# Optimization experiments

Hardware: AMD Instinct MI355X
Metric: run time of the kernel (lower is better)

## Reference

```python
import jax, jax.numpy as jnp
import numpy as np

B, T, E_DIM, H, J, V = 32, 1000, 512, 512, 512, 1024
BLANK = 0

def setup_inputs() -> dict:
    key = jax.random.key(0)
    ks = jax.random.split(key, 8)
    s = lambda k, shp, sc: jax.random.normal(k, shp, jnp.float32) * sc
    return {
        "encoder_output": jax.random.normal(ks[0], (B, T, E_DIM), jnp.float32),
        "embed": s(ks[1], (V, H), 0.02),
        "W_ih": s(ks[2], (H, 4 * H), 0.05),
        "W_hh": s(ks[3], (H, 4 * H), 0.05),
        "b_lstm": jnp.zeros((4 * H,), jnp.float32),
        "W_enc": s(ks[4], (E_DIM, J), 0.05),
        "W_dec": s(ks[5], (H, J), 0.05),
        "b_joint": jnp.zeros((J,), jnp.float32),
        "W_out": s(ks[6], (J, V), 0.05),
    }

def _lstm_step(tok, h, c, embed, W_ih, W_hh, b):
    # prediction network: embedding lookup + single-layer LSTM cell
    x = embed[tok]                                   # [B, H]
    gates = x @ W_ih + h @ W_hh + b                  # [B, 4H]
    i, f, g, o = jnp.split(gates, 4, axis=-1)
    c_new = jax.nn.sigmoid(f) * c + jax.nn.sigmoid(i) * jnp.tanh(g)
    h_new = jax.nn.sigmoid(o) * jnp.tanh(c_new)
    return h_new, c_new

def reference(encoder_output, embed, W_ih, W_hh, b_lstm, W_enc, W_dec, b_joint, W_out):
    # transducer_greedy_decode (beam_size <= 1 path), vectorized over batch,
    # sequential over encoder time steps via lax.scan.
    Bv = encoder_output.shape[0]
    h0 = jnp.zeros((Bv, H), encoder_output.dtype)
    c0 = jnp.zeros((Bv, H), encoder_output.dtype)
    tok0 = jnp.full((Bv,), BLANK, jnp.int32)
    # initial decoder call on blank token with zero hidden
    out_PN0, c1 = _lstm_step(tok0, h0, c0, embed, W_ih, W_hh, b_lstm)
    # precompute encoder projection of the joint (same math, one big GEMM)
    enc_proj = encoder_output @ W_enc                # [B, T, J]

    def step(carry, enc_t):
        out_PN, h, c, score = carry
        logits = jnp.tanh(enc_t + out_PN @ W_dec + b_joint) @ W_out   # [B, V]
        logp = jax.nn.log_softmax(logits, axis=-1)
        lp = jnp.max(logp, axis=-1)                  # best log-prob
        pos = jnp.argmax(logp, axis=-1)              # best token
        emit = pos != BLANK                          # hypotheses to update
        h_new, c_new = _lstm_step(pos.astype(jnp.int32), h, c, embed, W_ih, W_hh, b_lstm)
        m = emit[:, None]
        out_PN = jnp.where(m, h_new, out_PN)
        h = jnp.where(m, h_new, h)
        c = jnp.where(m, c_new, c)
        score = score + jnp.where(emit, lp, 0.0)
        tok = jnp.where(emit, pos, BLANK)            # BLANK marks 'no emission'
        return (out_PN, h, c, score), tok

    init = (out_PN0, out_PN0, c1, jnp.zeros((Bv,), encoder_output.dtype))
    (_, _, _, scores), toks = jax.lax.scan(step, init, jnp.swapaxes(enc_proj, 0, 1))
    predictions = toks.T                             # [B, T], BLANK = no emission
    mean_exp_score = jnp.exp(scores).mean()
    return predictions, scores, mean_exp_score
```

## Files before the change

### kernel.cpp

```cpp
#include <hip/hip_runtime.h>
#include <math.h>

#define BB 32
#define TT 1000
#define HH 512
#define JJ 512
#define VV 1024
#define G4 2048
#define NB 128
#define NT 1024
#define NGRP 16
#define BPG (NB / NGRP)

#define RLX __ATOMIC_RELAXED
#define AGT __HIP_MEMORY_SCOPE_AGENT

__device__ __align__(16) float g_encp[(size_t)TT * JJ * BB];
__device__ __align__(16) float g_E[(size_t)VV * G4];
__device__ __align__(16) float g_h[HH * BB];
__device__ __align__(16) float g_c[BB * HH];
__device__ __align__(16) float g_joint[JJ * BB];
__device__ __align__(16) float g_hW[BB * G4];
__device__ float g_pm[BB * NB];
__device__ float g_ps[BB * NB];
__device__ int   g_pa[BB * NB];
__device__ float g_score[BB];
__device__ int g_cnt[3 * 1024];
__device__ int g_top[3 * 64];
__device__ int g_gen[3 * 1024];

__device__ __forceinline__ void gbar_arrive(int grp, int ph, int tp1) {
    __syncthreads();
    if (threadIdx.x == 0) {
        int p = __hip_atomic_fetch_add(&g_cnt[ph * 1024 + grp * 64], 1, RLX, AGT);
        if (p == tp1 * BPG - 1) {
            int q = __hip_atomic_fetch_add(&g_top[ph * 64], 1, RLX, AGT);
            if (q == tp1 * NGRP - 1) {
#pragma unroll
                for (int i = 0; i < NGRP; ++i)
                    __hip_atomic_store(&g_gen[ph * 1024 + i * 64], tp1, RLX, AGT);
            }
        }
    }
}
__device__ __forceinline__ void gbar_wait(int grp, int ph, int tp1) {
    if (threadIdx.x == 0) {
        while (__hip_atomic_load(&g_gen[ph * 1024 + grp * 64], RLX, AGT) < tp1)
            __builtin_amdgcn_s_sleep(1);
    }
    __syncthreads();
}

__global__ __launch_bounds__(256) void k_encproj(const float* __restrict__ enc,
                                                 const float* __restrict__ Wenc) {
    __shared__ __align__(16) float x[BB * 512];
    const int t = blockIdx.x;
    for (int i = threadIdx.x; i < BB * 128; i += 256) {
        const int b = i >> 7, k4 = i & 127;
        *reinterpret_cast<float4*>(x + b * 512 + k4 * 4) =
            *reinterpret_cast<const float4*>(enc + ((size_t)(b * TT + t)) * 512 + k4 * 4);
    }
    __syncthreads();
    const int j = threadIdx.x;
    float acc0[BB], acc1[BB];
#pragma unroll
    for (int b = 0; b < BB; ++b) { acc0[b] = 0.f; acc1[b] = 0.f; }
    for (int k4 = 0; k4 < 128; ++k4) {
        const int k = k4 * 4;
        float w0[4], w1[4];
#pragma unroll
        for (int i = 0; i < 4; ++i) {
            w0[i] = Wenc[(size_t)(k + i) * JJ + j];
            w1[i] = Wenc[(size_t)(k + i) * JJ + j + 256];
        }
#pragma unroll
        for (int b = 0; b < BB; ++b) {
            const float4 xv = *reinterpret_cast<const float4*>(x + b * 512 + k);
            acc0[b] += xv.x * w0[0] + xv.y * w0[1] + xv.z * w0[2] + xv.w * w0[3];
            acc1[b] += xv.x * w1[0] + xv.y * w1[1] + xv.z * w1[2] + xv.w * w1[3];
        }
    }
    float* outt = g_encp + (size_t)t * JJ * BB;
#pragma unroll
    for (int b = 0; b < BB; ++b) {
        outt[j * BB + b]         = acc0[b];
        outt[(j + 256) * BB + b] = acc1[b];
    }
}

__global__ __launch_bounds__(256) void k_embproj(const float* __restrict__ emb,
                                                 const float* __restrict__ Wih) {
    __shared__ __align__(16) float x[BB * 512];
    const int v0 = (blockIdx.x >> 2) * 32;
    const int g0 = (blockIdx.x & 3) * 512;
    for (int i = threadIdx.x; i < BB * 128; i += 256) {
        const int b = i >> 7, k4 = i & 127;
        *reinterpret_cast<float4*>(x + b * 512 + k4 * 4) =
            *reinterpret_cast<const float4*>(emb + (size_t)(v0 + b) * 512 + k4 * 4);
    }
    __syncthreads();
    const int j = g0 + threadIdx.x;
    float acc0[BB], acc1[BB];
#pragma unroll
    for (int b = 0; b < BB; ++b) { acc0[b] = 0.f; acc1[b] = 0.f; }
    for (int k4 = 0; k4 < 128; ++k4) {
        const int k = k4 * 4;
        float w0[4], w1[4];
#pragma unroll
        for (int i = 0; i < 4; ++i) {
            w0[i] = Wih[(size_t)(k + i) * G4 + j];
            w1[i] = Wih[(size_t)(k + i) * G4 + j + 256];
        }
#pragma unroll
        for (int b = 0; b < BB; ++b) {
            const float4 xv = *reinterpret_cast<const float4*>(x + b * 512 + k);
            acc0[b] += xv.x * w0[0] + xv.y * w0[1] + xv.z * w0[2] + xv.w * w0[3];
            acc1[b] += xv.x * w1[0] + xv.y * w1[1] + xv.z * w1[2] + xv.w * w1[3];
        }
    }
#pragma unroll
    for (int b = 0; b < BB; ++b) {
        g_E[(size_t)(v0 + b) * G4 + j]       = acc0[b];
        g_E[(size_t)(v0 + b) * G4 + j + 256] = acc1[b];
    }
}

__global__ void k_init(const float* __restrict__ bl) {
    const int k = threadIdx.x;
    const float ig = g_E[k]        + bl[k];
    const float gg = g_E[1024 + k] + bl[1024 + k];
    const float og = g_E[1536 + k] + bl[1536 + k];
    const float si = 1.f / (1.f + expf(-ig));
    const float so = 1.f / (1.f + expf(-og));
    const float c1 = si * tanhf(gg);
    const float h1 = so * tanhf(c1);
    for (int b = 0; b < BB; ++b) {
        g_h[k * BB + b] = h1;
        g_c[b * HH + k] = c1;
    }
    if (k < BB) g_score[k] = 0.f;
    for (int i = k; i < 3 * 1024; i += 512) { g_cnt[i] = 0; g_gen[i] = 0; }
    if (k < 3 * 64) g_top[k] = 0;
}

template<int KN>
__device__ __forceinline__ void mv4(const float* __restrict__ w_lds, const int wpad,
                                    const int c0, const int k0,
                                    const float* __restrict__ x_lds,
                                    const int ks, const int b4, float acc[4][4]) {
#pragma unroll
    for (int c = 0; c < 4; ++c)
#pragma unroll
        for (int r = 0; r < 4; ++r) acc[c][r] = 0.f;
#pragma unroll 8
    for (int i = 0; i < KN; ++i) {
        const int k = k0 + i * 8 + ks;
        const float4 xv = *reinterpret_cast<const float4*>(x_lds + k * 32 + b4 * 4);
        const float4 wv = *reinterpret_cast<const float4*>(w_lds + k * wpad + c0);
        acc[0][0] += wv.x * xv.x; acc[0][1] += wv.x * xv.y; acc[0][2] += wv.x * xv.z; acc[0][3] += wv.x * xv.w;
        acc[1][0] += wv.y * xv.x; acc[1][1] += wv.y * xv.y; acc[1][2] += wv.y * xv.z; acc[1][3] += wv.y * xv.w;
        acc[2][0] += wv.z * xv.x; acc[2][1] += wv.z * xv.y; acc[2][2] += wv.z * xv.z; acc[2][3] += wv.z * xv.w;
        acc[3][0] += wv.w * xv.x; acc[3][1] += wv.w * xv.y; acc[3][2] += wv.w * xv.z; acc[3][3] += wv.w * xv.w;
    }
#pragma unroll
    for (int off = 8; off <= 32; off <<= 1)
#pragma unroll
        for (int c = 0; c < 4; ++c)
#pragma unroll
            for (int r = 0; r < 4; ++r) acc[c][r] += __shfl_xor(acc[c][r], off, 64);
}

__global__ __launch_bounds__(NT) void k_loop(const float* __restrict__ Wdec,
                                             const float* __restrict__ Wout,
                                             const float* __restrict__ Whh,
                                             const float* __restrict__ bj,
                                             const float* __restrict__ bl,
                                             float* __restrict__ out) {
    __shared__ __align__(16) float x_lds[512 * 32];
    __shared__ __align__(16) float wab_lds[512 * 20];
    __shared__ __align__(16) float wout_lds[512 * 12];
    __shared__ float part_lds[2 * 160];
    __shared__ float logit_lds[8 * 33];
    __shared__ float red_m[2], red_s[2];
    __shared__ int   red_a[2];

    const int blk = blockIdx.x, tid = threadIdx.x;
    const int grp = blk & (NGRP - 1);
    const int wv = tid >> 6, lane = tid & 63, ks = lane >> 3, b4 = lane & 7;

    for (int i = tid; i < 512 * 20; i += NT) {
        const int k = i / 20, c = i - k * 20;
        wab_lds[i] = (c < 16) ? Whh[(size_t)k * G4 + blk * 16 + c]
                              : Wdec[(size_t)k * JJ + blk * 4 + (c - 16)];
    }
    for (int i = tid; i < 512 * 12; i += NT) {
        const int k = i / 12, c = i - k * 12;
        wout_lds[i] = (c < 8) ? Wout[(size_t)k * VV + blk * 8 + c] : 0.f;
    }
    float bjr[4];
#pragma unroll
    for (int c = 0; c < 4; ++c) bjr[c] = bj[blk * 4 + c];
    __syncthreads();

    float acc[4][4];
    for (int t = 0; t < TT; ++t) {
        {
            float v[16];
#pragma unroll
            for (int p = 0; p < 16; ++p)
                v[p] = __hip_atomic_load(&g_h[tid + p * 1024], RLX, AGT);
#pragma unroll
            for (int p = 0; p < 16; ++p) x_lds[tid + p * 1024] = v[p];
        }
        __syncthreads();
        if (wv < 4) {
            mv4<64>(wab_lds, 20, wv * 4, 0, x_lds, ks, b4, acc);
            if (ks == 0) {
#pragma unroll
                for (int c = 0; c < 4; ++c)
#pragma unroll
                    for (int j = 0; j < 4; ++j)
                        __hip_atomic_store(&g_hW[(size_t)(b4 * 4 + j) * G4 + blk * 16 + wv * 4 + c],
                                           acc[c][j], RLX, AGT);
            }
        } else if (wv < 6) {
            mv4<32>(wab_lds, 20, 16, (wv - 4) * 256, x_lds, ks, b4, acc);
            if (wv == 5 && ks == 0) {
#pragma unroll
                for (int c = 0; c < 4; ++c)
#pragma unroll
                    for (int j = 0; j < 4; ++j)
                        part_lds[c * 33 + b4 * 4 + j] = acc[c][j];
            }
        }
        __syncthreads();
        if (wv == 4 && ks == 0) {
            const float* ep = g_encp + (size_t)t * JJ * BB + (size_t)blk * 4 * BB;
#pragma unroll
            for (int c = 0; c < 4; ++c) {
                const float4 ev = *reinterpret_cast<const float4*>(ep + c * BB + b4 * 4);
                const float evv[4] = { ev.x, ev.y, ev.z, ev.w };
#pragma unroll
                for (int j = 0; j < 4; ++j) {
                    const float u = acc[c][j] + part_lds[c * 33 + b4 * 4 + j] + evv[j] + bjr[c];
                    __hip_atomic_store(&g_joint[(blk * 4 + c) * BB + b4 * 4 + j],
                                       tanhf(u), RLX, AGT);
                }
            }
        }
        gbar_arrive(grp, 0, t + 1);
        gbar_wait(grp, 0, t + 1);

        {
            float v[16];
#pragma unroll
            for (int p = 0; p < 16; ++p)
                v[p] = __hip_atomic_load(&g_joint[tid + p * 1024], RLX, AGT);
#pragma unroll
            for (int p = 0; p < 16; ++p) x_lds[tid + p * 1024] = v[p];
        }
        __syncthreads();
        if (wv < 4) {
            const int tile = wv & 1, kh = wv >> 1;
            mv4<32>(wout_lds, 12, tile * 4, kh * 256, x_lds, ks, b4, acc);
            if (kh == 1 && ks == 0) {
#pragma unroll
                for (int c = 0; c < 4; ++c)
#pragma unroll
                    for (int j = 0; j < 4; ++j)
                        part_lds[tile * 160 + c * 33 + b4 * 4 + j] = acc[c][j];
            }
        }
        __syncthreads();
        if (wv < 2 && ks == 0) {
#pragma unroll
            for (int c = 0; c < 4; ++c)
#pragma unroll
                for (int j = 0; j < 4; ++j)
                    logit_lds[(wv * 4 + c) * 33 + b4 * 4 + j] =
                        acc[c][j] + part_lds[wv * 160 + c * 33 + b4 * 4 + j];
        }
        __syncthreads();
        if (wv == 0 && lane < BB) {
            const int b = lane;
            float m = -1e30f; int a = 0;
#pragma unroll
            for (int c = 0; c < 8; ++c) {
                const float l = logit_lds[c * 33 + b];
                if (l > m) { m = l; a = blk * 8 + c; }
            }
            float s = 0.f;
#pragma unroll
            for (int c = 0; c < 8; ++c) s += expf(logit_lds[c * 33 + b] - m);
            __hip_atomic_store(&g_pm[b * NB + blk], m, RLX, AGT);
            __hip_atomic_store(&g_pa[b * NB + blk], a, RLX, AGT);
            __hip_atomic_store(&g_ps[b * NB + blk], s, RLX, AGT);
        }
        gbar_arrive(grp, 1, t + 1);

        if (blk < BB) {
            gbar_wait(grp, 1, t + 1);
            const int r = blk;
            float m0 = -1e30f, s_loc = 0.f; int a0 = 1 << 30;
            if (tid < NB) {
                m0 = __hip_atomic_load(&g_pm[r * NB + tid], RLX, AGT);
                a0 = __hip_atomic_load(&g_pa[r * NB + tid], RLX, AGT);
                s_loc = __hip_atomic_load(&g_ps[r * NB + tid], RLX, AGT);
            }
            float m = m0; int a = a0;
#pragma unroll
            for (int off = 32; off; off >>= 1) {
                const float om = __shfl_xor(m, off, 64);
                const int   oa = __shfl_xor(a, off, 64);
                if (om > m || (om == m && oa < a)) { m = om; a = oa; }
            }
            if (lane == 0 && wv < 2) { red_m[wv] = m; red_a[wv] = a; }
            __syncthreads();
            float M; int P;
            {
                const float ma = red_m[0], mb = red_m[1];
                const int aa = red_a[0], ab = red_a[1];
                if (mb > ma || (mb == ma && ab < aa)) { M = mb; P = ab; }
                else { M = ma; P = aa; }
            }
            float e = (tid < NB) ? s_loc * expf(m0 - M) : 0.f;
#pragma unroll
            for (int off = 32; off; off >>= 1) e += __shfl_xor(e, off, 64);
            if (lane == 0 && wv < 2) red_s[wv] = e;
            __syncthreads();
            if (tid == 0) {
                const float S = red_s[0] + red_s[1];
                out[r * TT + t] = (float)P;
                if (P != 0) g_score[r] += -logf(S);
            }
            if (P != 0 && tid < HH) {
                const int k = tid;
                const float* Ep = g_E + (size_t)P * G4;
                const float hw0 = __hip_atomic_load(&g_hW[(size_t)r * G4 + k],        RLX, AGT);
                const float hw1 = __hip_atomic_load(&g_hW[(size_t)r * G4 + 512 + k],  RLX, AGT);
                const float hw2 = __hip_atomic_load(&g_hW[(size_t)r * G4 + 1024 + k], RLX, AGT);
                const float hw3 = __hip_atomic_load(&g_hW[(size_t)r * G4 + 1536 + k], RLX, AGT);
                const float i_g = Ep[k]        + hw0 + bl[k];
                const float f_g = Ep[512 + k]  + hw1 + bl[512 + k];
                const float g_g = Ep[1024 + k] + hw2 + bl[1024 + k];
                const float o_g = Ep[1536 + k] + hw3 + bl[1536 + k];
                const float si = 1.f / (1.f + expf(-i_g));
                const float sf = 1.f / (1.f + expf(-f_g));
                const float so = 1.f / (1.f + expf(-o_g));
                const float cn = sf * g_c[r * HH + k] + si * tanhf(g_g);
                const float hn = so * tanhf(cn);
                g_c[r * HH + k] = cn;
                __hip_atomic_store(&g_h[k * BB + r], hn, RLX, AGT);
            }
        }
        gbar_arrive(grp, 2, t + 1);
        gbar_wait(grp, 2, t + 1);
    }
}

__global__ void k_final(float* __restrict__ out) {
    const int b = threadIdx.x;
    float e = 0.f;
    if (b < BB) {
        const float sc = g_score[b];
        out[BB * TT + b] = sc;
        e = expf(sc);
    }
#pragma unroll
    for (int off = 32; off; off >>= 1) e += __shfl_xor(e, off, 64);
    if (b == 0) out[BB * TT + BB] = e / (float)BB;
}

extern "C" void kernel_launch(void* const* d_in, const int* in_sizes, int n_in,
                              void* d_out, int out_size, void* d_ws, size_t ws_size,
                              hipStream_t stream) {
    const float* enc  = (const float*)d_in[0];
    const float* emb  = (const float*)d_in[1];
    const float* Wih  = (const float*)d_in[2];
    const float* Whh  = (const float*)d_in[3];
    const float* bl   = (const float*)d_in[4];
    const float* Wenc = (const float*)d_in[5];
    const float* Wdec = (const float*)d_in[6];
    const float* bj   = (const float*)d_in[7];
    const float* Wout = (const float*)d_in[8];
    float* out = (float*)d_out;

    hipLaunchKernelGGL(k_encproj, dim3(TT), dim3(256), 0, stream, enc, Wenc);
    hipLaunchKernelGGL(k_embproj, dim3(128), dim3(256), 0, stream, emb, Wih);
    hipLaunchKernelGGL(k_init, dim3(1), dim3(512), 0, stream, bl);

    void* args[] = { (void*)&Wdec, (void*)&Wout, (void*)&Whh,
                     (void*)&bj, (void*)&bl, (void*)&out };
    hipLaunchCooperativeKernel((const void*)k_loop, dim3(NB), dim3(NT), args, 0, stream);

    hipLaunchKernelGGL(k_final, dim3(1), dim3(64), 0, stream, out);
}
```

Measured before the change: 28.17 ms.

## Replace hierarchical atomic grid barrier with flag-array barrier and spread LSTM update

Replaces the two-level counter-based grid barrier with a per-block flag array: each block writes its step number and then polls all 128 flags in parallel, taking the min with a block-wide reduction. This removes the serialized fetch_add chains and the generation broadcast. The LSTM update is now split across all 128 blocks (4 per batch row, each block doing 128 hidden units), where before only 32 blocks did it. Every block therefore repeats the argmax/logsumexp reduction for its row, and the W_dec matvec is spread over 4 waves with the encoder projection prefetched before the first sync. The cost is more polling traffic on 128 flags and redundant per-row reductions.

```diff
diff --git a/kernel.cpp b/kernel.cpp
--- a/kernel.cpp
+++ b/kernel.cpp
@@ -9,8 +9,6 @@
 #define G4 2048
 #define NB 128
 #define NT 1024
-#define NGRP 16
-#define BPG (NB / NGRP)
 
 #define RLX __ATOMIC_RELAXED
 #define AGT __HIP_MEMORY_SCOPE_AGENT
@@ -25,31 +23,7 @@
 __device__ float g_ps[BB * NB];
 __device__ int   g_pa[BB * NB];
 __device__ float g_score[BB];
-__device__ int g_cnt[3 * 1024];
-__device__ int g_top[3 * 64];
-__device__ int g_gen[3 * 1024];
-
-__device__ __forceinline__ void gbar_arrive(int grp, int ph, int tp1) {
-    __syncthreads();
-    if (threadIdx.x == 0) {
-        int p = __hip_atomic_fetch_add(&g_cnt[ph * 1024 + grp * 64], 1, RLX, AGT);
-        if (p == tp1 * BPG - 1) {
-            int q = __hip_atomic_fetch_add(&g_top[ph * 64], 1, RLX, AGT);
-            if (q == tp1 * NGRP - 1) {
-#pragma unroll
-                for (int i = 0; i < NGRP; ++i)
-                    __hip_atomic_store(&g_gen[ph * 1024 + i * 64], tp1, RLX, AGT);
-            }
-        }
-    }
-}
-__device__ __forceinline__ void gbar_wait(int grp, int ph, int tp1) {
-    if (threadIdx.x == 0) {
-        while (__hip_atomic_load(&g_gen[ph * 1024 + grp * 64], RLX, AGT) < tp1)
-            __builtin_amdgcn_s_sleep(1);
-    }
-    __syncthreads();
-}
+__device__ int g_arr[3][NB];
 
 __global__ __launch_bounds__(256) void k_encproj(const float* __restrict__ enc,
                                                  const float* __restrict__ Wenc) {
@@ -139,8 +113,7 @@
         g_c[b * HH + k] = c1;
     }
     if (k < BB) g_score[k] = 0.f;
-    for (int i = k; i < 3 * 1024; i += 512) { g_cnt[i] = 0; g_gen[i] = 0; }
-    if (k < 3 * 64) g_top[k] = 0;
+    if (k < 3 * NB) ((int*)g_arr)[k] = 0;
 }
 
 template<int KN>
@@ -179,14 +152,16 @@
     __shared__ __align__(16) float x_lds[512 * 32];
     __shared__ __align__(16) float wab_lds[512 * 20];
     __shared__ __align__(16) float wout_lds[512 * 12];
-    __shared__ float part_lds[2 * 160];
+    __shared__ float part_lds[560];
     __shared__ float logit_lds[8 * 33];
     __shared__ float red_m[2], red_s[2];
     __shared__ int   red_a[2];
+    __shared__ int   red_bar[2];
+    __shared__ int   bar_done;
 
     const int blk = blockIdx.x, tid = threadIdx.x;
-    const int grp = blk & (NGRP - 1);
     const int wv = tid >> 6, lane = tid & 63, ks = lane >> 3, b4 = lane & 7;
+    const int row = blk >> 2, qs = blk & 3;
 
     for (int i = tid; i < 512 * 20; i += NT) {
         const int k = i / 20, c = i - k * 20;
@@ -204,6 +179,7 @@
 
     float acc[4][4];
     for (int t = 0; t < TT; ++t) {
+        const int tp1 = t + 1;
         {
             float v[16];
 #pragma unroll
@@ -211,6 +187,12 @@
                 v[p] = __hip_atomic_load(&g_h[tid + p * 1024], RLX, AGT);
 #pragma unroll
             for (int p = 0; p < 16; ++p) x_lds[tid + p * 1024] = v[p];
+        }
+        float encr[4];
+        if (wv == 8 && lane < 32) {
+            const float* ep = g_encp + (size_t)t * JJ * BB + (size_t)blk * 4 * BB;
+#pragma unroll
+            for (int c = 0; c < 4; ++c) encr[c] = ep[c * BB + lane];
         }
         __syncthreads();
         if (wv < 4) {
@@ -223,33 +205,41 @@
                         __hip_atomic_store(&g_hW[(size_t)(b4 * 4 + j) * G4 + blk * 16 + wv * 4 + c],
                                            acc[c][j], RLX, AGT);
             }
-        } else if (wv < 6) {
-            mv4<32>(wab_lds, 20, 16, (wv - 4) * 256, x_lds, ks, b4, acc);
-            if (wv == 5 && ks == 0) {
+        } else if (wv < 8) {
+            mv4<16>(wab_lds, 20, 16, (wv - 4) * 128, x_lds, ks, b4, acc);
+            if (ks == 0) {
 #pragma unroll
                 for (int c = 0; c < 4; ++c)
 #pragma unroll
                     for (int j = 0; j < 4; ++j)
-                        part_lds[c * 33 + b4 * 4 + j] = acc[c][j];
-            }
-        }
-        __syncthreads();
-        if (wv == 4 && ks == 0) {
-            const float* ep = g_encp + (size_t)t * JJ * BB + (size_t)blk * 4 * BB;
+                        part_lds[(wv - 4) * 136 + c * 33 + b4 * 4 + j] = acc[c][j];
+            }
+        }
+        __syncthreads();
+        if (wv == 8 && lane < 32) {
+            const int b = lane;
 #pragma unroll
             for (int c = 0; c < 4; ++c) {
-                const float4 ev = *reinterpret_cast<const float4*>(ep + c * BB + b4 * 4);
-                const float evv[4] = { ev.x, ev.y, ev.z, ev.w };
-#pragma unroll
-                for (int j = 0; j < 4; ++j) {
-                    const float u = acc[c][j] + part_lds[c * 33 + b4 * 4 + j] + evv[j] + bjr[c];
-                    __hip_atomic_store(&g_joint[(blk * 4 + c) * BB + b4 * 4 + j],
-                                       tanhf(u), RLX, AGT);
-                }
-            }
-        }
-        gbar_arrive(grp, 0, t + 1);
-        gbar_wait(grp, 0, t + 1);
+                const float u = part_lds[c * 33 + b] + part_lds[136 + c * 33 + b]
+                              + part_lds[272 + c * 33 + b] + part_lds[408 + c * 33 + b]
+                              + encr[c] + bjr[c];
+                __hip_atomic_store(&g_joint[(blk * 4 + c) * BB + b], tanhf(u), RLX, AGT);
+            }
+        }
+        __syncthreads();
+        if (tid == 0) __hip_atomic_store(&g_arr[0][blk], tp1, RLX, AGT);
+        for (;;) {
+            int m = 0x7fffffff;
+            if (tid < NB) m = __hip_atomic_load(&g_arr[0][tid], RLX, AGT);
+#pragma unroll
+            for (int off = 32; off; off >>= 1) m = min(m, __shfl_xor(m, off, 64));
+            if (lane == 0 && wv < 2) red_bar[wv] = m;
+            __syncthreads();
+            if (tid == 0) bar_done = (min(red_bar[0], red_bar[1]) >= tp1);
+            __syncthreads();
+            if (bar_done) break;
+            __builtin_amdgcn_s_sleep(1);
+        }
 
         {
             float v[16];
@@ -296,16 +286,27 @@
             __hip_atomic_store(&g_pa[b * NB + blk], a, RLX, AGT);
             __hip_atomic_store(&g_ps[b * NB + blk], s, RLX, AGT);
         }
-        gbar_arrive(grp, 1, t + 1);
-
-        if (blk < BB) {
-            gbar_wait(grp, 1, t + 1);
-            const int r = blk;
-            float m0 = -1e30f, s_loc = 0.f; int a0 = 1 << 30;
+        __syncthreads();
+        if (tid == 0) __hip_atomic_store(&g_arr[1][blk], tp1, RLX, AGT);
+        for (;;) {
+            int m = 0x7fffffff;
+            if (tid < NB) m = __hip_atomic_load(&g_arr[1][tid], RLX, AGT);
+#pragma unroll
+            for (int off = 32; off; off >>= 1) m = min(m, __shfl_xor(m, off, 64));
+            if (lane == 0 && wv < 2) red_bar[wv] = m;
+            __syncthreads();
+            if (tid == 0) bar_done = (min(red_bar[0], red_bar[1]) >= tp1);
+            __syncthreads();
+            if (bar_done) break;
+            __builtin_amdgcn_s_sleep(1);
+        }
+
+        {
+            float m0 = -1e30f, s0 = 0.f; int a0 = 1 << 30;
             if (tid < NB) {
-                m0 = __hip_atomic_load(&g_pm[r * NB + tid], RLX, AGT);
-                a0 = __hip_atomic_load(&g_pa[r * NB + tid], RLX, AGT);
-                s_loc = __hip_atomic_load(&g_ps[r * NB + tid], RLX, AGT);
+                m0 = __hip_atomic_load(&g_pm[row * NB + tid], RLX, AGT);
+                a0 = __hip_atomic_load(&g_pa[row * NB + tid], RLX, AGT);
+                s0 = __hip_atomic_load(&g_ps[row * NB + tid], RLX, AGT);
             }
             float m = m0; int a = a0;
 #pragma unroll
@@ -323,23 +324,22 @@
                 if (mb > ma || (mb == ma && ab < aa)) { M = mb; P = ab; }
                 else { M = ma; P = aa; }
             }
-            float e = (tid < NB) ? s_loc * expf(m0 - M) : 0.f;
+            float e = (tid < NB) ? s0 * expf(m0 - M) : 0.f;
 #pragma unroll
             for (int off = 32; off; off >>= 1) e += __shfl_xor(e, off, 64);
             if (lane == 0 && wv < 2) red_s[wv] = e;
             __syncthreads();
-            if (tid == 0) {
-                const float S = red_s[0] + red_s[1];
-                out[r * TT + t] = (float)P;
-                if (P != 0) g_score[r] += -logf(S);
-            }
-            if (P != 0 && tid < HH) {
-                const int k = tid;
+            if (qs == 0 && tid == 0) {
+                out[row * TT + t] = (float)P;
+                if (P != 0) g_score[row] += -logf(red_s[0] + red_s[1]);
+            }
+            if (P != 0 && tid < 128) {
+                const int k = qs * 128 + tid;
                 const float* Ep = g_E + (size_t)P * G4;
-                const float hw0 = __hip_atomic_load(&g_hW[(size_t)r * G4 + k],        RLX, AGT);
-                const float hw1 = __hip_atomic_load(&g_hW[(size_t)r * G4 + 512 + k],  RLX, AGT);
-                const float hw2 = __hip_atomic_load(&g_hW[(size_t)r * G4 + 1024 + k], RLX, AGT);
-                const float hw3 = __hip_atomic_load(&g_hW[(size_t)r * G4 + 1536 + k], RLX, AGT);
+                const float hw0 = __hip_atomic_load(&g_hW[(size_t)row * G4 + k],        RLX, AGT);
+                const float hw1 = __hip_atomic_load(&g_hW[(size_t)row * G4 + 512 + k],  RLX, AGT);
+                const float hw2 = __hip_atomic_load(&g_hW[(size_t)row * G4 + 1024 + k], RLX, AGT);
+                const float hw3 = __hip_atomic_load(&g_hW[(size_t)row * G4 + 1536 + k], RLX, AGT);
                 const float i_g = Ep[k]        + hw0 + bl[k];
                 const float f_g = Ep[512 + k]  + hw1 + bl[512 + k];
                 const float g_g = Ep[1024 + k] + hw2 + bl[1024 + k];
@@ -347,14 +347,26 @@
                 const float si = 1.f / (1.f + expf(-i_g));
                 const float sf = 1.f / (1.f + expf(-f_g));
                 const float so = 1.f / (1.f + expf(-o_g));
-                const float cn = sf * g_c[r * HH + k] + si * tanhf(g_g);
+                const float cn = sf * g_c[row * HH + k] + si * tanhf(g_g);
                 const float hn = so * tanhf(cn);
-                g_c[r * HH + k] = cn;
-                __hip_atomic_store(&g_h[k * BB + r], hn, RLX, AGT);
-            }
-        }
-        gbar_arrive(grp, 2, t + 1);
-        gbar_wait(grp, 2, t + 1);
+                g_c[row * HH + k] = cn;
+                __hip_atomic_store(&g_h[k * BB + row], hn, RLX, AGT);
+            }
+        }
+        __syncthreads();
+        if (tid == 0) __hip_atomic_store(&g_arr[2][blk], tp1, RLX, AGT);
+        for (;;) {
+            int m = 0x7fffffff;
+            if (tid < NB) m = __hip_atomic_load(&g_arr[2][tid], RLX, AGT);
+#pragma unroll
+            for (int off = 32; off; off >>= 1) m = min(m, __shfl_xor(m, off, 64));
+            if (lane == 0 && wv < 2) red_bar[wv] = m;
+            __syncthreads();
+            if (tid == 0) bar_done = (min(red_bar[0], red_bar[1]) >= tp1);
+            __syncthreads();
+            if (bar_done) break;
+            __builtin_amdgcn_s_sleep(1);
+        }
     }
 }
 
```

Result: slower. 31.77 ms (+12.8%).
